# Performance work log

Hardware: AMD Instinct MI355X
Metric: run time of the kernel (lower is better)

Reference implementation:

```python
import jax, jax.numpy as jnp
import numpy as np

L, D, H, FF = 6, 1024, 16, 4096
HD = D // H
EPS = 1e-5


def _ln(x, g, b):
    m = jnp.mean(x, axis=-1, keepdims=True)
    v = jnp.var(x, axis=-1, keepdims=True)
    return (x - m) * jax.lax.rsqrt(v + EPS) * g + b


def _heads(t, S, B):  # [S,B,D] -> [B*H,S,HD]
    return t.reshape(S, B * H, HD).swapaxes(0, 1)


def _attn(q, k, v, mask):
    # q,k,v: [B*H, Sq/Sk, HD]; q pre-scaled
    scores = jnp.einsum('bqd,bkd->bqk', q, k)
    if mask is not None:
        scores = scores + mask  # broadcast [1,Sq,Sk]
    p = jax.nn.softmax(scores, axis=-1)
    return jnp.einsum('bqk,bkd->bqd', p, v)


def _self_attn(x, w_qkv, b_qkv, w_out, b_out, mask):
    S, B, _ = x.shape
    qkv = x @ w_qkv.T + b_qkv  # [S,B,3D]
    q, k, v = jnp.split(qkv, 3, axis=-1)
    q = q * (HD ** -0.5)
    a = _attn(_heads(q, S, B), _heads(k, S, B), _heads(v, S, B), mask)
    a = a.swapaxes(0, 1).reshape(S, B, D)
    return a @ w_out.T + b_out


def _cross_attn(x, mem, w_q, b_q, w_kv, b_kv, w_out, b_out):
    S, B, _ = x.shape
    Sm = mem.shape[0]
    q = (x @ w_q.T + b_q) * (HD ** -0.5)
    kv = mem @ w_kv.T + b_kv  # [Sm,B,2D]
    k, v = jnp.split(kv, 2, axis=-1)
    a = _attn(_heads(q, S, B), _heads(k, Sm, B), _heads(v, Sm, B), None)
    a = a.swapaxes(0, 1).reshape(S, B, D)
    return a @ w_out.T + b_out


def _ffn(x, w1, b1, w2, b2):
    h = jax.nn.gelu(x @ w1.T + b1, approximate=False)
    return h @ w2.T + b2


def setup_inputs() -> dict:
    key = jax.random.key(0)
    ks = iter(jax.random.split(key, 64))
    def p(*shape, s=0.02):
        return (jax.random.normal(next(ks), shape, dtype=jnp.float32) * s)
    inp = {
        'src': jax.random.normal(next(ks), (512, 8, D), dtype=jnp.float32),
        'tgt': jax.random.normal(next(ks), (512, 8, D), dtype=jnp.float32),
        # encoder params (stacked over L layers)
        'enc_qkv_w': p(L, 3 * D, D), 'enc_qkv_b': p(L, 3 * D),
        'enc_out_w': p(L, D, D), 'enc_out_b': p(L, D),
        'enc_ln1_g': jnp.ones((L, D)), 'enc_ln1_b': jnp.zeros((L, D)),
        'enc_fc1_w': p(L, FF, D), 'enc_fc1_b': p(L, FF),
        'enc_fc2_w': p(L, D, FF), 'enc_fc2_b': p(L, D),
        'enc_ln2_g': jnp.ones((L, D)), 'enc_ln2_b': jnp.zeros((L, D)),
        'enc_norm_g': jnp.ones((D,)), 'enc_norm_b': jnp.zeros((D,)),
        # decoder params
        'dec_qkv_w': p(L, 3 * D, D), 'dec_qkv_b': p(L, 3 * D),
        'dec_sout_w': p(L, D, D), 'dec_sout_b': p(L, D),
        'dec_ln1_g': jnp.ones((L, D)), 'dec_ln1_b': jnp.zeros((L, D)),
        'dec_q_w': p(L, D, D), 'dec_q_b': p(L, D),
        'dec_kv_w': p(L, 2 * D, D), 'dec_kv_b': p(L, 2 * D),
        'dec_cout_w': p(L, D, D), 'dec_cout_b': p(L, D),
        'dec_ln2_g': jnp.ones((L, D)), 'dec_ln2_b': jnp.zeros((L, D)),
        'dec_fc1_w': p(L, FF, D), 'dec_fc1_b': p(L, FF),
        'dec_fc2_w': p(L, D, FF), 'dec_fc2_b': p(L, D),
        'dec_ln3_g': jnp.ones((L, D)), 'dec_ln3_b': jnp.zeros((L, D)),
        'dec_norm_g': jnp.ones((D,)), 'dec_norm_b': jnp.zeros((D,)),
    }
    return inp


def reference(src, tgt,
              enc_qkv_w, enc_qkv_b, enc_out_w, enc_out_b,
              enc_ln1_g, enc_ln1_b, enc_fc1_w, enc_fc1_b,
              enc_fc2_w, enc_fc2_b, enc_ln2_g, enc_ln2_b,
              enc_norm_g, enc_norm_b,
              dec_qkv_w, dec_qkv_b, dec_sout_w, dec_sout_b,
              dec_ln1_g, dec_ln1_b, dec_q_w, dec_q_b,
              dec_kv_w, dec_kv_b, dec_cout_w, dec_cout_b,
              dec_ln2_g, dec_ln2_b, dec_fc1_w, dec_fc1_b,
              dec_fc2_w, dec_fc2_b, dec_ln3_g, dec_ln3_b,
              dec_norm_g, dec_norm_b):
    St = tgt.shape[0]
    # causal additive mask [1,St,St]
    causal = jnp.where(jnp.tril(jnp.ones((St, St), dtype=bool)), 0.0, -jnp.inf)
    causal = causal[None].astype(src.dtype)

    # ---- encoder ----
    x = src
    for i in range(L):
        x = x + _self_attn(_ln(x, enc_ln1_g[i], enc_ln1_b[i]),
                           enc_qkv_w[i], enc_qkv_b[i], enc_out_w[i], enc_out_b[i], None)
        x = x + _ffn(_ln(x, enc_ln2_g[i], enc_ln2_b[i]),
                     enc_fc1_w[i], enc_fc1_b[i], enc_fc2_w[i], enc_fc2_b[i])
    memory = _ln(x, enc_norm_g, enc_norm_b)

    # ---- decoder ----
    y = tgt
    for i in range(L):
        y = y + _self_attn(_ln(y, dec_ln1_g[i], dec_ln1_b[i]),
                           dec_qkv_w[i], dec_qkv_b[i], dec_sout_w[i], dec_sout_b[i], causal)
        y = y + _cross_attn(_ln(y, dec_ln2_g[i], dec_ln2_b[i]), memory,
                            dec_q_w[i], dec_q_b[i], dec_kv_w[i], dec_kv_b[i],
                            dec_cout_w[i], dec_cout_b[i])
        y = y + _ffn(_ln(y, dec_ln3_g[i], dec_ln3_b[i]),
                     dec_fc1_w[i], dec_fc1_b[i], dec_fc2_w[i], dec_fc2_b[i])
    return _ln(y, dec_norm_g, dec_norm_b)
```

## Files before the change

### kernel.cpp

```cpp
#include <hip/hip_runtime.h>

typedef __attribute__((ext_vector_type(4))) float f32x4;
typedef __attribute__((ext_vector_type(8))) short short8;
typedef unsigned int u32;
typedef unsigned short u16;
typedef __attribute__((ext_vector_type(2))) u32 u32x2;
typedef __attribute__((ext_vector_type(4))) u32 u32x4;

#define DEV __device__ __forceinline__
#define SB0  __builtin_amdgcn_sched_barrier(0)
#define HBAR asm volatile("s_barrier" ::: "memory")

DEV u16 f2b(float f){
  u32 u = __builtin_bit_cast(u32, f);
  u32 r = u + 0x7fffu + ((u >> 16) & 1u);
  return (u16)(r >> 16);
}
DEV u32 pk2(float a, float b){ return (u32)f2b(a) | ((u32)f2b(b) << 16); }

DEV void gload16(const void* g, void* l){
  __builtin_amdgcn_global_load_lds((const __attribute__((address_space(1))) void*)g,
                                   (__attribute__((address_space(3))) void*)l, 16, 0, 0);
}
DEV u32 lds_addr(void* p){
  return (u32)(unsigned long long)(__attribute__((address_space(3))) char*)p;
}

__global__ __launch_bounds__(256) void cvt_k(const float* __restrict__ in,
                                             u16* __restrict__ out, int n8)
{
  int i = blockIdx.x*256 + threadIdx.x;
  const int stride = gridDim.x*256;
  for (; i < n8; i += stride){
    const float4 a = ((const float4*)in)[2*i];
    const float4 b = ((const float4*)in)[2*i+1];
    u32x4 r;
    r.x = pk2(a.x,a.y); r.y = pk2(a.z,a.w);
    r.z = pk2(b.x,b.y); r.w = pk2(b.z,b.w);
    ((u32x4*)out)[i] = r;
  }
}

template<int OUT_F32>
__global__ __launch_bounds__(256) void ln_k(const float* __restrict__ x,
    const float* __restrict__ gam, const float* __restrict__ bet,
    void* __restrict__ out)
{
  const int row = blockIdx.x, tid = threadIdx.x;
  const float4 v = ((const float4*)(x + row*1024))[tid];
  float s = (v.x + v.y) + (v.z + v.w);
  float q = (v.x*v.x + v.y*v.y) + (v.z*v.z + v.w*v.w);
  #pragma unroll
  for (int m = 1; m < 64; m <<= 1){ s += __shfl_xor(s, m); q += __shfl_xor(q, m); }
  __shared__ float ps[4], pq[4];
  if ((tid & 63) == 0){ ps[tid>>6] = s; pq[tid>>6] = q; }
  __syncthreads();
  s = (ps[0]+ps[1]) + (ps[2]+ps[3]);
  q = (pq[0]+pq[1]) + (pq[2]+pq[3]);
  const float mean = s * (1.f/1024.f);
  const float var  = q * (1.f/1024.f) - mean*mean;
  const float rstd = rsqrtf(var + 1e-5f);
  const float4 gg = ((const float4*)gam)[tid];
  const float4 bb = ((const float4*)bet)[tid];
  const float o0 = (v.x-mean)*rstd*gg.x + bb.x;
  const float o1 = (v.y-mean)*rstd*gg.y + bb.y;
  const float o2 = (v.z-mean)*rstd*gg.z + bb.z;
  const float o3 = (v.w-mean)*rstd*gg.w + bb.w;
  if (OUT_F32){
    float4 r; r.x=o0; r.y=o1; r.z=o2; r.w=o3;
    ((float4*)out)[row*256 + tid] = r;
  } else {
    u32x2 r; r.x = pk2(o0,o1); r.y = pk2(o2,o3);
    ((u32x2*)out)[row*256 + tid] = r;
  }
}

template<int DO_GELU>
__global__ __launch_bounds__(512,2) void gemm256_k(
    const u16* __restrict__ A, const u16* __restrict__ W,
    const float* __restrict__ bias, u16* __restrict__ Cout,
    int M, int N, int K)
{
  __shared__ char lds[131072];
  const int tid = threadIdx.x;
  const int lane = tid & 63, wid = tid >> 6;
  const int wr = wid >> 2, wc = wid & 3;
  const int g = lane >> 4, c16 = lane & 15;

  const u32 nwg = gridDim.x * gridDim.y;
  u32 flat = blockIdx.x + gridDim.x * blockIdx.y;
  {
    const u32 q = nwg >> 3, r = nwg & 7;
    const u32 xcd = flat & 7, idx = flat >> 3;
    flat = (xcd < r ? xcd*(q+1) : r*(q+1) + (xcd-r)*q) + idx;
  }
  const int m0 = (int)(flat % gridDim.x) * 256;
  const int n0 = (int)(flat / gridDim.x) * 256;

  f32x4 acc[8][4];
  #pragma unroll
  for (int m = 0; m < 8; m++)
    #pragma unroll
    for (int n = 0; n < 4; n++) acc[m][n] = (f32x4){0.f,0.f,0.f,0.f};

  const int srow = tid >> 3, schk = tid & 7;
  const int scg = schk ^ (srow & 7);
  const u16* aS = A + (size_t)(m0 + srow)*K + scg*8;
  const u16* wS = W + (size_t)(n0 + srow)*K + scg*8;

  auto SG = [&](const u16* base, int regionOff, int sb, int half, int i, int kk){
    gload16(base + (size_t)(half*128 + i*64)*K + kk,
            lds + sb*65536 + regionOff + half*16384 + i*8192 + tid*16);
  };
  short8 af[4][2], bf[4][2];
  auto LDA4 = [&](char* bufA, int mbase){
    #pragma unroll
    for (int i = 0; i < 4; i++){
      const int r = (mbase + i)*16 + c16;
      const int rx = r & 7;
      af[i][0] = *(const short8*)(bufA + r*128 + ((g ^ rx) << 4));
      af[i][1] = *(const short8*)(bufA + r*128 + (((4 + g) ^ rx) << 4));
    }
  };
  auto LDB2 = [&](char* bufB, int nbase){
    #pragma unroll
    for (int i = 0; i < 2; i++){
      const int r = (wc & 1)*64 + (nbase + i)*16 + c16;
      const int rx = r & 7;
      bf[nbase+i][0] = *(const short8*)(bufB + r*128 + ((g ^ rx) << 4));
      bf[nbase+i][1] = *(const short8*)(bufB + r*128 + (((4 + g) ^ rx) << 4));
    }
  };

  const int NT = K >> 6;
  SG(wS, 32768, 0, 0, 0, 0); SG(wS, 32768, 0, 0, 1, 0);
  SG(wS, 32768, 0, 1, 0, 0); SG(wS, 32768, 0, 1, 1, 0);
  SG(aS, 0,     0, 0, 0, 0); SG(aS, 0,     0, 0, 1, 0);
  SG(aS, 0,     0, 1, 0, 0); SG(aS, 0,     0, 1, 1, 0);
  asm volatile("s_waitcnt vmcnt(1)" ::: "memory");
  HBAR;

  for (int t = 0; t < NT; ++t){
    const int b = t & 1, sb = b ^ 1;
    const int skk = (t+1) << 6;
    const bool st = (t+1 < NT);
    char* bufA = lds + b*65536 + wr*16384;
    char* bufB = lds + b*65536 + 32768 + (wc >> 1)*16384;

    LDA4(bufA, 0); LDB2(bufB, 0);
    if (st){ SG(wS, 32768, sb, 0, 0, skk); SG(wS, 32768, sb, 0, 1, skk); }
    HBAR;
    asm volatile("s_waitcnt lgkmcnt(0)" ::: "memory"); SB0;
    __builtin_amdgcn_s_setprio(1);
    #pragma unroll
    for (int ks = 0; ks < 2; ks++)
      #pragma unroll
      for (int i = 0; i < 4; i++)
        #pragma unroll
        for (int j = 0; j < 2; j++)
          acc[i][j] = __builtin_amdgcn_mfma_f32_16x16x32_bf16(af[i][ks], bf[j][ks], acc[i][j], 0,0,0);
    __builtin_amdgcn_s_setprio(0);
    LDB2(bufB, 2);
    if (st){ SG(wS, 32768, sb, 1, 0, skk); SG(wS, 32768, sb, 1, 1, skk); }
    HBAR;
    asm volatile("s_waitcnt lgkmcnt(0)" ::: "memory"); SB0;
    __builtin_amdgcn_s_setprio(1);
    #pragma unroll
    for (int ks = 0; ks < 2; ks++)
      #pragma unroll
      for (int i = 0; i < 4; i++)
        #pragma unroll
        for (int j = 2; j < 4; j++)
          acc[i][j] = __builtin_amdgcn_mfma_f32_16x16x32_bf16(af[i][ks], bf[j][ks], acc[i][j], 0,0,0);
    __builtin_amdgcn_s_setprio(0);
    if (st) asm volatile("s_waitcnt vmcnt(4)" ::: "memory");
    else    asm volatile("s_waitcnt vmcnt(0)" ::: "memory");
    HBAR;
    LDA4(bufA, 4);
    if (st){ SG(aS, 0, sb, 0, 0, skk); SG(aS, 0, sb, 0, 1, skk); }
    asm volatile("s_waitcnt lgkmcnt(0)" ::: "memory"); SB0;
    __builtin_amdgcn_s_setprio(1);
    #pragma unroll
    for (int ks = 0; ks < 2; ks++)
      #pragma unroll
      for (int i = 0; i < 4; i++)
        #pragma unroll
        for (int j = 0; j < 2; j++)
          acc[4+i][j] = __builtin_amdgcn_mfma_f32_16x16x32_bf16(af[i][ks], bf[j][ks], acc[4+i][j], 0,0,0);
    __builtin_amdgcn_s_setprio(0);
    if (st){ SG(aS, 0, sb, 1, 0, skk); SG(aS, 0, sb, 1, 1, skk); }
    HBAR;
    __builtin_amdgcn_s_setprio(1);
    #pragma unroll
    for (int ks = 0; ks < 2; ks++)
      #pragma unroll
      for (int i = 0; i < 4; i++)
        #pragma unroll
        for (int j = 2; j < 4; j++)
          acc[4+i][j] = __builtin_amdgcn_mfma_f32_16x16x32_bf16(af[i][ks], bf[j][ks], acc[4+i][j], 0,0,0);
    __builtin_amdgcn_s_setprio(0);
    if (st) asm volatile("s_waitcnt vmcnt(1)" ::: "memory");
    HBAR;
  }

  #pragma unroll
  for (int n = 0; n < 4; n++){
    const int col = n0 + wc*64 + n*16 + c16;
    const float bv = bias[col];
    #pragma unroll
    for (int m = 0; m < 8; m++){
      const int rbase = m0 + wr*128 + m*16 + g*4;
      #pragma unroll
      for (int r = 0; r < 4; r++){
        float v = acc[m][n][r] + bv;
        if (DO_GELU) v = 0.5f*v*(1.f + erff(v*0.70710678118654752f));
        Cout[(size_t)(rbase + r)*N + col] = f2b(v);
      }
    }
  }
}

template<int DO_GELU, int DO_RES, int OUT_F32>
__global__ __launch_bounds__(256,2) void gemm_k(
    const u16* __restrict__ A, const u16* __restrict__ W,
    const float* __restrict__ bias, const float* __restrict__ res,
    void* __restrict__ Cout, int M, int N, int K)
{
  __shared__ char sA[16384];
  __shared__ char sB[16384];
  const int tid = threadIdx.x;
  const int lane = tid & 63, w = tid >> 6;
  const int wr = w >> 1, wc = w & 1;
  const int g = lane >> 4, c16 = lane & 15;

  const u32 nwg = gridDim.x * gridDim.y;
  u32 flat = blockIdx.x + gridDim.x * blockIdx.y;
  {
    const u32 q = nwg >> 3, r = nwg & 7;
    const u32 xcd = flat & 7, idx = flat >> 3;
    flat = (xcd < r ? xcd*(q+1) : r*(q+1) + (xcd-r)*q) + idx;
  }
  const int m0 = (int)(flat % gridDim.x) * 128;
  const int n0 = (int)(flat / gridDim.x) * 128;

  f32x4 acc[4][4];
  #pragma unroll
  for (int m = 0; m < 4; m++)
    #pragma unroll
    for (int n = 0; n < 4; n++) acc[m][n] = (f32x4){0.f,0.f,0.f,0.f};

  const int arow = tid >> 3, achk = tid & 7;
  const int acg = achk ^ (arow & 7);
  const u16* aSrc = A + (size_t)(m0 + arow)*K + acg*8;
  const u16* wSrc = W + (size_t)(n0 + arow)*K + acg*8;
  char* aDst = sA + w*1024;
  char* bDst = sB + w*1024;

  for (int kk = 0; kk < K; kk += 64){
    __syncthreads();
    #pragma unroll
    for (int i = 0; i < 4; i++){
      gload16(aSrc + (size_t)i*32*K + kk, aDst + i*4096);
      gload16(wSrc + (size_t)i*32*K + kk, bDst + i*4096);
    }
    __syncthreads();
    #pragma unroll
    for (int ks = 0; ks < 2; ks++){
      short8 af[4], bf[4];
      #pragma unroll
      for (int m = 0; m < 4; m++){
        const int row = wr*64 + m*16 + c16;
        af[m] = *(const short8*)(sA + row*128 + (((ks*4 + g) ^ (row & 7)) << 4));
      }
      #pragma unroll
      for (int n = 0; n < 4; n++){
        const int row = wc*64 + n*16 + c16;
        bf[n] = *(const short8*)(sB + row*128 + (((ks*4 + g) ^ (row & 7)) << 4));
      }
      #pragma unroll
      for (int m = 0; m < 4; m++)
        #pragma unroll
        for (int n = 0; n < 4; n++)
          acc[m][n] = __builtin_amdgcn_mfma_f32_16x16x32_bf16(af[m], bf[n], acc[m][n], 0,0,0);
    }
  }
  #pragma unroll
  for (int n = 0; n < 4; n++){
    const int col = n0 + wc*64 + n*16 + c16;
    const float bv = bias[col];
    #pragma unroll
    for (int m = 0; m < 4; m++){
      const int rbase = m0 + wr*64 + m*16 + g*4;
      #pragma unroll
      for (int r = 0; r < 4; r++){
        float v = acc[m][n][r] + bv;
        if (DO_GELU) v = 0.5f*v*(1.f + erff(v*0.70710678118654752f));
        if (DO_RES)  v += res[(size_t)(rbase + r)*N + col];
        if (OUT_F32) ((float*)Cout)[(size_t)(rbase + r)*N + col] = v;
        else         ((u16*)Cout)[(size_t)(rbase + r)*N + col] = f2b(v);
      }
    }
  }
}

template<int DO_GELU, int DO_RES, int OUT_F32>
__global__ __launch_bounds__(256,2) void gemm64_k(
    const u16* __restrict__ A, const u16* __restrict__ W,
    const float* __restrict__ bias, const float* __restrict__ res,
    void* __restrict__ Cout, int M, int N, int K)
{
  __shared__ char sA[8192];
  __shared__ char sB[8192];
  const int tid = threadIdx.x;
  const int lane = tid & 63, w = tid >> 6;
  const int wr = w >> 1, wc = w & 1;
  const int g = lane >> 4, c16 = lane & 15;

  const u32 nwg = gridDim.x * gridDim.y;
  u32 flat = blockIdx.x + gridDim.x * blockIdx.y;
  {
    const u32 q = nwg >> 3, r = nwg & 7;
    const u32 xcd = flat & 7, idx = flat >> 3;
    flat = (xcd < r ? xcd*(q+1) : r*(q+1) + (xcd-r)*q) + idx;
  }
  const int m0 = (int)(flat % gridDim.x) * 64;
  const int n0 = (int)(flat / gridDim.x) * 64;

  f32x4 acc[2][2];
  #pragma unroll
  for (int m = 0; m < 2; m++)
    #pragma unroll
    for (int n = 0; n < 2; n++) acc[m][n] = (f32x4){0.f,0.f,0.f,0.f};

  const int arow = tid >> 3, achk = tid & 7;
  const int acg = achk ^ (arow & 7);
  const u16* aSrc = A + (size_t)(m0 + arow)*K + acg*8;
  const u16* wSrc = W + (size_t)(n0 + arow)*K + acg*8;
  char* aDst = sA + w*1024;
  char* bDst = sB + w*1024;

  for (int kk = 0; kk < K; kk += 64){
    __syncthreads();
    #pragma unroll
    for (int i = 0; i < 2; i++){
      gload16(aSrc + (size_t)i*32*K + kk, aDst + i*4096);
      gload16(wSrc + (size_t)i*32*K + kk, bDst + i*4096);
    }
    __syncthreads();
    #pragma unroll
    for (int ks = 0; ks < 2; ks++){
      short8 af[2], bf[2];
      #pragma unroll
      for (int m = 0; m < 2; m++){
        const int row = wr*32 + m*16 + c16;
        af[m] = *(const short8*)(sA + row*128 + (((ks*4 + g) ^ (row & 7)) << 4));
      }
      #pragma unroll
      for (int n = 0; n < 2; n++){
        const int row = wc*32 + n*16 + c16;
        bf[n] = *(const short8*)(sB + row*128 + (((ks*4 + g) ^ (row & 7)) << 4));
      }
      #pragma unroll
      for (int m = 0; m < 2; m++)
        #pragma unroll
        for (int n = 0; n < 2; n++)
          acc[m][n] = __builtin_amdgcn_mfma_f32_16x16x32_bf16(af[m], bf[n], acc[m][n], 0,0,0);
    }
  }
  #pragma unroll
  for (int n = 0; n < 2; n++){
    const int col = n0 + wc*32 + n*16 + c16;
    const float bv = bias[col];
    #pragma unroll
    for (int m = 0; m < 2; m++){
      const int rbase = m0 + wr*32 + m*16 + g*4;
      #pragma unroll
      for (int r = 0; r < 4; r++){
        float v = acc[m][n][r] + bv;
        if (DO_GELU) v = 0.5f*v*(1.f + erff(v*0.70710678118654752f));
        if (DO_RES)  v += res[(size_t)(rbase + r)*N + col];
        if (OUT_F32) ((float*)Cout)[(size_t)(rbase + r)*N + col] = v;
        else         ((u16*)Cout)[(size_t)(rbase + r)*N + col] = f2b(v);
      }
    }
  }
}

template<int CAUSAL>
__global__ __launch_bounds__(256,2) void attn_k(
    const u16* __restrict__ Qb, int qB, int qS,
    const u16* __restrict__ Kb, int kB, int kS,
    const u16* __restrict__ Vb, int vB, int vS,
    u16* __restrict__ Ob, int oB, int oS, float scale)
{
  __shared__ char smem[16384];
  const int tid = threadIdx.x;
  const int lane = tid & 63, w = tid >> 6;
  const int g = lane >> 4, c16 = lane & 15;
  const int qt = blockIdx.x, bh = blockIdx.y;
  const int b = bh >> 4, h = bh & 15;
  const u16* Q  = Qb + b*qB + h*64;
  const u16* Kp = Kb + b*kB + h*64;
  const u16* Vp = Vb + b*vB + h*64;
  u16*       Op = Ob + b*oB + h*64;

  const int qrow = qt*64 + w*16 + c16;
  const short8 bq0 = *(const short8*)(Q + qrow*qS + g*8);
  const short8 bq1 = *(const short8*)(Q + qrow*qS + 32 + g*8);

  f32x4 o[4];
  #pragma unroll
  for (int d = 0; d < 4; d++) o[d] = (f32x4){0.f,0.f,0.f,0.f};
  float mrun = -__builtin_inff(), lrun = 0.f;

  const int srow = tid >> 3, schk = tid & 7;
  const u16* kSrc = Kp + srow*kS + (schk ^ (srow & 7))*8;
  const u16* vSrc = Vp + srow*vS + schk*8;
  const u32 vtr0 = lds_addr(smem) + 8192 + (8*g + (c16 >> 2))*128 + (c16 & 3)*8;

  auto STAGE = [&](int p, int j0){
    gload16(kSrc + (size_t)j0*kS, smem + p*4096 + w*1024);
    gload16(vSrc + (size_t)j0*vS, smem + 8192 + p*4096 + w*1024);
  };
  auto COMPUTE = [&](int p, int j0){
    char* Ks = smem + p*4096;
    f32x4 st[2];
    #pragma unroll
    for (int t = 0; t < 2; t++){
      const int row = t*16 + c16;
      const int rx = row & 7;
      const short8 ka0 = *(const short8*)(Ks + row*128 + ((g ^ rx) << 4));
      const short8 ka1 = *(const short8*)(Ks + row*128 + (((4 + g) ^ rx) << 4));
      f32x4 z = (f32x4){0.f,0.f,0.f,0.f};
      z = __builtin_amdgcn_mfma_f32_16x16x32_bf16(ka0, bq0, z, 0,0,0);
      z = __builtin_amdgcn_mfma_f32_16x16x32_bf16(ka1, bq1, z, 0,0,0);
      st[t] = z;
    }
    float mloc = -__builtin_inff();
    #pragma unroll
    for (int t = 0; t < 2; t++)
      #pragma unroll
      for (int r = 0; r < 4; r++){
        float sv = st[t][r]*scale;
        if (CAUSAL){ if (j0 + t*16 + g*4 + r > qrow) sv = -__builtin_inff(); }
        st[t][r] = sv;
        mloc = fmaxf(mloc, sv);
      }
    mloc = fmaxf(mloc, __shfl_xor(mloc, 16));
    mloc = fmaxf(mloc, __shfl_xor(mloc, 32));
    const float mnew = fmaxf(mrun, mloc);
    const float corr = __expf(mrun - mnew);
    float psum = 0.f;
    u32 pk00, pk01, pk10, pk11;
    {
      float p0 = __expf(st[0][0]-mnew), p1 = __expf(st[0][1]-mnew);
      float p2 = __expf(st[0][2]-mnew), p3 = __expf(st[0][3]-mnew);
      psum += (p0+p1) + (p2+p3);
      pk00 = pk2(p0,p1); pk01 = pk2(p2,p3);
      p0 = __expf(st[1][0]-mnew); p1 = __expf(st[1][1]-mnew);
      p2 = __expf(st[1][2]-mnew); p3 = __expf(st[1][3]-mnew);
      psum += (p0+p1) + (p2+p3);
      pk10 = pk2(p0,p1); pk11 = pk2(p2,p3);
    }
    psum += __shfl_xor(psum, 16);
    psum += __shfl_xor(psum, 32);
    lrun = lrun*corr + psum;
    mrun = mnew;
    #pragma unroll
    for (int d = 0; d < 4; d++){
      o[d][0]*=corr; o[d][1]*=corr; o[d][2]*=corr; o[d][3]*=corr;
    }
    const int sl0 = c16 | (((g << 1)     & 3) << 4);
    const int sl1 = c16 | ((((g << 1)+1) & 3) << 4);
    const u32 a00 = (u32)__shfl((int)pk00, sl0), a01 = (u32)__shfl((int)pk01, sl0);
    const u32 a02 = (u32)__shfl((int)pk00, sl1), a03 = (u32)__shfl((int)pk01, sl1);
    const u32 a10 = (u32)__shfl((int)pk10, sl0), a11 = (u32)__shfl((int)pk11, sl0);
    const u32 a12 = (u32)__shfl((int)pk10, sl1), a13 = (u32)__shfl((int)pk11, sl1);
    const bool hi = g >= 2;
    union { short8 s; u32 u[4]; } pb;
    pb.u[0] = hi ? a10 : a00;
    pb.u[1] = hi ? a11 : a01;
    pb.u[2] = hi ? a12 : a02;
    pb.u[3] = hi ? a13 : a03;

    const u32 vtr = vtr0 + p*4096;
    u32x2 t00,t01,t10,t11,t20,t21,t30,t31;
    asm volatile("ds_read_b64_tr_b16 %0, %1 offset:0"   : "=v"(t00) : "v"(vtr));
    asm volatile("ds_read_b64_tr_b16 %0, %1 offset:512" : "=v"(t01) : "v"(vtr));
    asm volatile("ds_read_b64_tr_b16 %0, %1 offset:32"  : "=v"(t10) : "v"(vtr));
    asm volatile("ds_read_b64_tr_b16 %0, %1 offset:544" : "=v"(t11) : "v"(vtr));
    asm volatile("ds_read_b64_tr_b16 %0, %1 offset:64"  : "=v"(t20) : "v"(vtr));
    asm volatile("ds_read_b64_tr_b16 %0, %1 offset:576" : "=v"(t21) : "v"(vtr));
    asm volatile("ds_read_b64_tr_b16 %0, %1 offset:96"  : "=v"(t30) : "v"(vtr));
    asm volatile("ds_read_b64_tr_b16 %0, %1 offset:608" : "=v"(t31) : "v"(vtr));
    asm volatile("s_waitcnt lgkmcnt(0)" ::: "memory");
    __builtin_amdgcn_sched_barrier(0);
    union { short8 s; u32x2 d[2]; } v0u, v1u, v2u, v3u;
    v0u.d[0]=t00; v0u.d[1]=t01;
    v1u.d[0]=t10; v1u.d[1]=t11;
    v2u.d[0]=t20; v2u.d[1]=t21;
    v3u.d[0]=t30; v3u.d[1]=t31;
    o[0] = __builtin_amdgcn_mfma_f32_16x16x32_bf16(v0u.s, pb.s, o[0], 0,0,0);
    o[1] = __builtin_amdgcn_mfma_f32_16x16x32_bf16(v1u.s, pb.s, o[1], 0,0,0);
    o[2] = __builtin_amdgcn_mfma_f32_16x16x32_bf16(v2u.s, pb.s, o[2], 0,0,0);
    o[3] = __builtin_amdgcn_mfma_f32_16x16x32_bf16(v3u.s, pb.s, o[3], 0,0,0);
  };

  const int nCh = CAUSAL ? (2*qt + 2) : 16;
  STAGE(0, 0);
  for (int jc = 0; jc < nCh - 1; ++jc){
    STAGE((jc+1) & 1, (jc+1)*32);
    asm volatile("s_waitcnt vmcnt(2)" ::: "memory");
    HBAR; SB0;
    COMPUTE(jc & 1, jc*32);
    SB0; HBAR;
  }
  asm volatile("s_waitcnt vmcnt(0)" ::: "memory");
  HBAR; SB0;
  COMPUTE((nCh-1) & 1, (nCh-1)*32);
  SB0; HBAR;

  const float inv = 1.f / lrun;
  char* Olds = smem;
  #pragma unroll
  for (int dd = 0; dd < 4; dd++){
    u32x2 val;
    val.x = pk2(o[dd][0]*inv, o[dd][1]*inv);
    val.y = pk2(o[dd][2]*inv, o[dd][3]*inv);
    const int row = w*16 + c16;
    const int off = 32*dd + 8*g;
    const int chunk = off >> 4, rem = off & 15;
    *(u32x2*)(Olds + row*128 + ((chunk ^ (row & 7)) << 4) + rem) = val;
  }
  __syncthreads();
  const int orow = tid >> 2, oc = tid & 3;
  #pragma unroll
  for (int i = 0; i < 2; i++){
    const int ch = oc*2 + i;
    const u32x4 vv = *(const u32x4*)(Olds + orow*128 + ((ch ^ (orow & 7)) << 4));
    *(u32x4*)(Op + (qt*64 + orow)*oS + ch*8) = vv;
  }
}

static inline int cvt_grid(int n8){ int g = (n8 + 255) / 256; return g > 2048 ? 2048 : g; }

extern "C" void kernel_launch(void* const* d_in, const int* in_sizes, int n_in,
                              void* d_out, int out_size, void* d_ws, size_t ws_size,
                              hipStream_t stream)
{
  (void)in_sizes; (void)n_in; (void)out_size; (void)ws_size;
  const float* src      = (const float*)d_in[0];
  const float* tgt      = (const float*)d_in[1];
  const float* e_qkv_w  = (const float*)d_in[2];
  const float* e_qkv_b  = (const float*)d_in[3];
  const float* e_out_w  = (const float*)d_in[4];
  const float* e_out_b  = (const float*)d_in[5];
  const float* e_ln1_g  = (const float*)d_in[6];
  const float* e_ln1_b  = (const float*)d_in[7];
  const float* e_fc1_w  = (const float*)d_in[8];
  const float* e_fc1_b  = (const float*)d_in[9];
  const float* e_fc2_w  = (const float*)d_in[10];
  const float* e_fc2_b  = (const float*)d_in[11];
  const float* e_ln2_g  = (const float*)d_in[12];
  const float* e_ln2_b  = (const float*)d_in[13];
  const float* e_nrm_g  = (const float*)d_in[14];
  const float* e_nrm_b  = (const float*)d_in[15];
  const float* dc_qkv_w = (const float*)d_in[16];
  const float* dc_qkv_b = (const float*)d_in[17];
  const float* dc_sout_w= (const float*)d_in[18];
  const float* dc_sout_b= (const float*)d_in[19];
  const float* dc_ln1_g = (const float*)d_in[20];
  const float* dc_ln1_b = (const float*)d_in[21];
  const float* dc_q_w   = (const float*)d_in[22];
  const float* dc_q_b   = (const float*)d_in[23];
  const float* dc_kv_w  = (const float*)d_in[24];
  const float* dc_kv_b  = (const float*)d_in[25];
  const float* dc_cout_w= (const float*)d_in[26];
  const float* dc_cout_b= (const float*)d_in[27];
  const float* dc_ln2_g = (const float*)d_in[28];
  const float* dc_ln2_b = (const float*)d_in[29];
  const float* dc_fc1_w = (const float*)d_in[30];
  const float* dc_fc1_b = (const float*)d_in[31];
  const float* dc_fc2_w = (const float*)d_in[32];
  const float* dc_fc2_b = (const float*)d_in[33];
  const float* dc_ln3_g = (const float*)d_in[34];
  const float* dc_ln3_b = (const float*)d_in[35];
  const float* dc_nrm_g = (const float*)d_in[36];
  const float* dc_nrm_b = (const float*)d_in[37];

  char* ws = (char*)d_ws;
  u16*  ln_out = (u16*)(ws);
  u16*  attn_o = (u16*)(ws + (8u<<20));
  u16*  membuf = (u16*)(ws + (16u<<20));
  float* xres  = (float*)(ws + (24u<<20));
  u16*  region = (u16*)(ws + (40u<<20));
  u16*  qkv   = region;
  u16*  hbuf  = region;
  u16*  qbuf  = region;
  u16*  kvbuf = region + (4u<<20);

  const dim3 blk(256);
  const dim3 blk512(512);
  const int M = 4096;

  u16* wb = (u16*)(ws + (72u<<20));
  size_t woff = 0;
  auto CV = [&](const float* wsrc, size_t n)->u16* {
    u16* p = wb + woff; woff += n;
    cvt_k<<<cvt_grid((int)(n >> 3)), blk, 0, stream>>>(wsrc, p, (int)(n >> 3));
    return p;
  };
  u16* Weqkv = CV(e_qkv_w,  6ull*3072*1024);
  u16* Weout = CV(e_out_w,  6ull*1024*1024);
  u16* Wefc1 = CV(e_fc1_w,  6ull*4096*1024);
  u16* Wefc2 = CV(e_fc2_w,  6ull*4096*1024);
  u16* Wdqkv = CV(dc_qkv_w, 6ull*3072*1024);
  u16* Wdsout= CV(dc_sout_w,6ull*1024*1024);
  u16* Wdq   = CV(dc_q_w,   6ull*1024*1024);
  u16* Wdkv  = CV(dc_kv_w,  6ull*2048*1024);
  u16* Wdcout= CV(dc_cout_w,6ull*1024*1024);
  u16* Wdfc1 = CV(dc_fc1_w, 6ull*4096*1024);
  u16* Wdfc2 = CV(dc_fc2_w, 6ull*4096*1024);

  for (int i = 0; i < 6; i++){
    const float* xin = i ? xres : src;
    ln_k<0><<<4096, blk, 0, stream>>>(xin, e_ln1_g + i*1024, e_ln1_b + i*1024, ln_out);
    gemm256_k<0><<<dim3(16, 12), blk512, 0, stream>>>(ln_out,
        Weqkv + (size_t)i*3145728, e_qkv_b + i*3072, qkv, M, 3072, 1024);
    attn_k<0><<<dim3(8,128), blk, 0, stream>>>(qkv, 3072, 24576,
        qkv+1024, 3072, 24576, qkv+2048, 3072, 24576, attn_o, 1024, 8192, 0.125f);
    gemm64_k<0,1,1><<<dim3(64, 16), blk, 0, stream>>>(attn_o,
        Weout + (size_t)i*1048576, e_out_b + i*1024, xin, xres, M, 1024, 1024);
    ln_k<0><<<4096, blk, 0, stream>>>(xres, e_ln2_g + i*1024, e_ln2_b + i*1024, ln_out);
    gemm256_k<1><<<dim3(16, 16), blk512, 0, stream>>>(ln_out,
        Wefc1 + (size_t)i*4194304, e_fc1_b + i*4096, hbuf, M, 4096, 1024);
    gemm64_k<0,1,1><<<dim3(64, 16), blk, 0, stream>>>(hbuf,
        Wefc2 + (size_t)i*4194304, e_fc2_b + i*1024, xres, xres, M, 1024, 4096);
  }
  ln_k<0><<<4096, blk, 0, stream>>>(xres, e_nrm_g, e_nrm_b, membuf);

  for (int i = 0; i < 6; i++){
    const float* yin = i ? xres : tgt;
    ln_k<0><<<4096, blk, 0, stream>>>(yin, dc_ln1_g + i*1024, dc_ln1_b + i*1024, ln_out);
    gemm256_k<0><<<dim3(16, 12), blk512, 0, stream>>>(ln_out,
        Wdqkv + (size_t)i*3145728, dc_qkv_b + i*3072, qkv, M, 3072, 1024);
    attn_k<1><<<dim3(8,128), blk, 0, stream>>>(qkv, 3072, 24576,
        qkv+1024, 3072, 24576, qkv+2048, 3072, 24576, attn_o, 1024, 8192, 0.125f);
    gemm64_k<0,1,1><<<dim3(64, 16), blk, 0, stream>>>(attn_o,
        Wdsout + (size_t)i*1048576, dc_sout_b + i*1024, yin, xres, M, 1024, 1024);
    ln_k<0><<<4096, blk, 0, stream>>>(xres, dc_ln2_g + i*1024, dc_ln2_b + i*1024, ln_out);
    gemm64_k<0,0,0><<<dim3(64, 16), blk, 0, stream>>>(ln_out,
        Wdq + (size_t)i*1048576, dc_q_b + i*1024, nullptr, qbuf, M, 1024, 1024);
    gemm64_k<0,0,0><<<dim3(64, 32), blk, 0, stream>>>(membuf,
        Wdkv + (size_t)i*2097152, dc_kv_b + i*2048, nullptr, kvbuf, M, 2048, 1024);
    attn_k<0><<<dim3(8,128), blk, 0, stream>>>(qbuf, 1024, 8192,
        kvbuf, 2048, 16384, kvbuf+1024, 2048, 16384, attn_o, 1024, 8192, 0.125f);
    gemm64_k<0,1,1><<<dim3(64, 16), blk, 0, stream>>>(attn_o,
        Wdcout + (size_t)i*1048576, dc_cout_b + i*1024, xres, xres, M, 1024, 1024);
    ln_k<0><<<4096, blk, 0, stream>>>(xres, dc_ln3_g + i*1024, dc_ln3_b + i*1024, ln_out);
    gemm256_k<1><<<dim3(16, 16), blk512, 0, stream>>>(ln_out,
        Wdfc1 + (size_t)i*4194304, dc_fc1_b + i*4096, hbuf, M, 4096, 1024);
    gemm64_k<0,1,1><<<dim3(64, 16), blk, 0, stream>>>(hbuf,
        Wdfc2 + (size_t)i*4194304, dc_fc2_b + i*1024, xres, xres, M, 1024, 4096);
  }
  ln_k<1><<<4096, blk, 0, stream>>>(xres, dc_nrm_g, dc_nrm_b, d_out);
}
```

Baseline: 3.615 ms.

## Replace 64x64 GEMM with double-buffered 128x128 pipelined 8-wave kernel

Replaces the 64x64-tile single-buffered GEMM used for the N=1024/2048 projections with a new 128x128-tile kernel that uses 512 threads (8 waves), double-buffered LDS (64KB), and prefetches the next K-tile via global_load_lds while computing on the current one. It uses explicit waitcnt and barriers, splits A-fragment loads into two halves, and raises MFMA priority with setprio. The aim is to hide global-load latency and improve data reuse per tile. In exchange the grid drops to 256 or 512 workgroups, which may underfill the GPU's compute units for the 1024-wide outputs.

```diff
diff --git a/kernel.cpp b/kernel.cpp
--- a/kernel.cpp
+++ b/kernel.cpp
@@ -221,16 +221,15 @@
 }
 
 template<int DO_GELU, int DO_RES, int OUT_F32>
-__global__ __launch_bounds__(256,2) void gemm_k(
+__global__ __launch_bounds__(512,2) void gemm128p_k(
     const u16* __restrict__ A, const u16* __restrict__ W,
     const float* __restrict__ bias, const float* __restrict__ res,
     void* __restrict__ Cout, int M, int N, int K)
 {
-  __shared__ char sA[16384];
-  __shared__ char sB[16384];
+  __shared__ char lds[65536];
   const int tid = threadIdx.x;
-  const int lane = tid & 63, w = tid >> 6;
-  const int wr = w >> 1, wc = w & 1;
+  const int lane = tid & 63, wid = tid >> 6;
+  const int wr = wid >> 2, wc = wid & 3;
   const int g = lane >> 4, c16 = lane & 15;
 
   const u32 nwg = gridDim.x * gridDim.y;
@@ -243,137 +242,89 @@
   const int m0 = (int)(flat % gridDim.x) * 128;
   const int n0 = (int)(flat / gridDim.x) * 128;
 
-  f32x4 acc[4][4];
+  f32x4 acc[4][2];
   #pragma unroll
   for (int m = 0; m < 4; m++)
     #pragma unroll
-    for (int n = 0; n < 4; n++) acc[m][n] = (f32x4){0.f,0.f,0.f,0.f};
-
-  const int arow = tid >> 3, achk = tid & 7;
-  const int acg = achk ^ (arow & 7);
-  const u16* aSrc = A + (size_t)(m0 + arow)*K + acg*8;
-  const u16* wSrc = W + (size_t)(n0 + arow)*K + acg*8;
-  char* aDst = sA + w*1024;
-  char* bDst = sB + w*1024;
-
-  for (int kk = 0; kk < K; kk += 64){
-    __syncthreads();
-    #pragma unroll
-    for (int i = 0; i < 4; i++){
-      gload16(aSrc + (size_t)i*32*K + kk, aDst + i*4096);
-      gload16(wSrc + (size_t)i*32*K + kk, bDst + i*4096);
-    }
-    __syncthreads();
-    #pragma unroll
-    for (int ks = 0; ks < 2; ks++){
-      short8 af[4], bf[4];
-      #pragma unroll
-      for (int m = 0; m < 4; m++){
-        const int row = wr*64 + m*16 + c16;
-        af[m] = *(const short8*)(sA + row*128 + (((ks*4 + g) ^ (row & 7)) << 4));
-      }
-      #pragma unroll
-      for (int n = 0; n < 4; n++){
-        const int row = wc*64 + n*16 + c16;
-        bf[n] = *(const short8*)(sB + row*128 + (((ks*4 + g) ^ (row & 7)) << 4));
-      }
-      #pragma unroll
-      for (int m = 0; m < 4; m++)
+    for (int n = 0; n < 2; n++) acc[m][n] = (f32x4){0.f,0.f,0.f,0.f};
+
+  const int srow = tid >> 3, schk = tid & 7;
+  const int scg = schk ^ (srow & 7);
+  const u16* aS = A + (size_t)(m0 + srow)*K + scg*8;
+  const u16* wS = W + (size_t)(n0 + srow)*K + scg*8;
+
+  auto SG = [&](const u16* base, int regionOff, int sb, int i, int kk){
+    gload16(base + (size_t)(i*64)*K + kk,
+            lds + sb*32768 + regionOff + i*8192 + tid*16);
+  };
+  short8 af[2][2], af2[2][2], bf[2][2];
+  auto LDA = [&](short8 (*dst)[2], char* bufA, int mbase){
+    #pragma unroll
+    for (int i = 0; i < 2; i++){
+      const int r = wr*64 + (mbase + i)*16 + c16;
+      const int rx = r & 7;
+      dst[i][0] = *(const short8*)(bufA + r*128 + ((g ^ rx) << 4));
+      dst[i][1] = *(const short8*)(bufA + r*128 + (((4 + g) ^ rx) << 4));
+    }
+  };
+  auto LDB = [&](char* bufB){
+    #pragma unroll
+    for (int i = 0; i < 2; i++){
+      const int r = wc*32 + i*16 + c16;
+      const int rx = r & 7;
+      bf[i][0] = *(const short8*)(bufB + r*128 + ((g ^ rx) << 4));
+      bf[i][1] = *(const short8*)(bufB + r*128 + (((4 + g) ^ rx) << 4));
+    }
+  };
+
+  const int NT = K >> 6;
+  SG(wS, 16384, 0, 0, 0); SG(wS, 16384, 0, 1, 0);
+  SG(aS, 0,     0, 0, 0); SG(aS, 0,     0, 1, 0);
+
+  for (int t = 0; t < NT; ++t){
+    const int b = t & 1, sb = b ^ 1;
+    const int skk = (t+1) << 6;
+    const bool st = (t+1 < NT);
+    char* bufA = lds + b*32768;
+    char* bufB = lds + b*32768 + 16384;
+
+    if (st){ SG(wS, 16384, sb, 0, skk); SG(wS, 16384, sb, 1, skk); }
+    if (st) asm volatile("s_waitcnt vmcnt(2)" ::: "memory");
+    else    asm volatile("s_waitcnt vmcnt(0)" ::: "memory");
+    HBAR;
+    LDA(af, bufA, 0); LDB(bufB);
+    if (st){ SG(aS, 0, sb, 0, skk); SG(aS, 0, sb, 1, skk); }
+    asm volatile("s_waitcnt lgkmcnt(0)" ::: "memory"); SB0;
+    __builtin_amdgcn_s_setprio(1);
+    #pragma unroll
+    for (int ks = 0; ks < 2; ks++)
+      #pragma unroll
+      for (int i = 0; i < 2; i++)
         #pragma unroll
-        for (int n = 0; n < 4; n++)
-          acc[m][n] = __builtin_amdgcn_mfma_f32_16x16x32_bf16(af[m], bf[n], acc[m][n], 0,0,0);
-    }
-  }
-  #pragma unroll
-  for (int n = 0; n < 4; n++){
-    const int col = n0 + wc*64 + n*16 + c16;
-    const float bv = bias[col];
-    #pragma unroll
-    for (int m = 0; m < 4; m++){
-      const int rbase = m0 + wr*64 + m*16 + g*4;
-      #pragma unroll
-      for (int r = 0; r < 4; r++){
-        float v = acc[m][n][r] + bv;
-        if (DO_GELU) v = 0.5f*v*(1.f + erff(v*0.70710678118654752f));
-        if (DO_RES)  v += res[(size_t)(rbase + r)*N + col];
-        if (OUT_F32) ((float*)Cout)[(size_t)(rbase + r)*N + col] = v;
-        else         ((u16*)Cout)[(size_t)(rbase + r)*N + col] = f2b(v);
-      }
-    }
-  }
-}
-
-template<int DO_GELU, int DO_RES, int OUT_F32>
-__global__ __launch_bounds__(256,2) void gemm64_k(
-    const u16* __restrict__ A, const u16* __restrict__ W,
-    const float* __restrict__ bias, const float* __restrict__ res,
-    void* __restrict__ Cout, int M, int N, int K)
-{
-  __shared__ char sA[8192];
-  __shared__ char sB[8192];
-  const int tid = threadIdx.x;
-  const int lane = tid & 63, w = tid >> 6;
-  const int wr = w >> 1, wc = w & 1;
-  const int g = lane >> 4, c16 = lane & 15;
-
-  const u32 nwg = gridDim.x * gridDim.y;
-  u32 flat = blockIdx.x + gridDim.x * blockIdx.y;
-  {
-    const u32 q = nwg >> 3, r = nwg & 7;
-    const u32 xcd = flat & 7, idx = flat >> 3;
-    flat = (xcd < r ? xcd*(q+1) : r*(q+1) + (xcd-r)*q) + idx;
-  }
-  const int m0 = (int)(flat % gridDim.x) * 64;
-  const int n0 = (int)(flat / gridDim.x) * 64;
-
-  f32x4 acc[2][2];
-  #pragma unroll
-  for (int m = 0; m < 2; m++)
-    #pragma unroll
-    for (int n = 0; n < 2; n++) acc[m][n] = (f32x4){0.f,0.f,0.f,0.f};
-
-  const int arow = tid >> 3, achk = tid & 7;
-  const int acg = achk ^ (arow & 7);
-  const u16* aSrc = A + (size_t)(m0 + arow)*K + acg*8;
-  const u16* wSrc = W + (size_t)(n0 + arow)*K + acg*8;
-  char* aDst = sA + w*1024;
-  char* bDst = sB + w*1024;
-
-  for (int kk = 0; kk < K; kk += 64){
-    __syncthreads();
-    #pragma unroll
-    for (int i = 0; i < 2; i++){
-      gload16(aSrc + (size_t)i*32*K + kk, aDst + i*4096);
-      gload16(wSrc + (size_t)i*32*K + kk, bDst + i*4096);
-    }
-    __syncthreads();
-    #pragma unroll
-    for (int ks = 0; ks < 2; ks++){
-      short8 af[2], bf[2];
-      #pragma unroll
-      for (int m = 0; m < 2; m++){
-        const int row = wr*32 + m*16 + c16;
-        af[m] = *(const short8*)(sA + row*128 + (((ks*4 + g) ^ (row & 7)) << 4));
-      }
-      #pragma unroll
-      for (int n = 0; n < 2; n++){
-        const int row = wc*32 + n*16 + c16;
-        bf[n] = *(const short8*)(sB + row*128 + (((ks*4 + g) ^ (row & 7)) << 4));
-      }
-      #pragma unroll
-      for (int m = 0; m < 2; m++)
+        for (int j = 0; j < 2; j++)
+          acc[i][j] = __builtin_amdgcn_mfma_f32_16x16x32_bf16(af[i][ks], bf[j][ks], acc[i][j], 0,0,0);
+    __builtin_amdgcn_s_setprio(0);
+    LDA(af2, bufA, 2);
+    asm volatile("s_waitcnt lgkmcnt(0)" ::: "memory"); SB0;
+    __builtin_amdgcn_s_setprio(1);
+    #pragma unroll
+    for (int ks = 0; ks < 2; ks++)
+      #pragma unroll
+      for (int i = 0; i < 2; i++)
         #pragma unroll
-        for (int n = 0; n < 2; n++)
-          acc[m][n] = __builtin_amdgcn_mfma_f32_16x16x32_bf16(af[m], bf[n], acc[m][n], 0,0,0);
-    }
-  }
+        for (int j = 0; j < 2; j++)
+          acc[2+i][j] = __builtin_amdgcn_mfma_f32_16x16x32_bf16(af2[i][ks], bf[j][ks], acc[2+i][j], 0,0,0);
+    __builtin_amdgcn_s_setprio(0);
+    HBAR;
+  }
+
   #pragma unroll
   for (int n = 0; n < 2; n++){
     const int col = n0 + wc*32 + n*16 + c16;
     const float bv = bias[col];
     #pragma unroll
-    for (int m = 0; m < 2; m++){
-      const int rbase = m0 + wr*32 + m*16 + g*4;
+    for (int m = 0; m < 4; m++){
+      const int rbase = m0 + wr*64 + m*16 + g*4;
       #pragma unroll
       for (int r = 0; r < 4; r++){
         float v = acc[m][n][r] + bv;
@@ -629,12 +580,12 @@
         Weqkv + (size_t)i*3145728, e_qkv_b + i*3072, qkv, M, 3072, 1024);
     attn_k<0><<<dim3(8,128), blk, 0, stream>>>(qkv, 3072, 24576,
         qkv+1024, 3072, 24576, qkv+2048, 3072, 24576, attn_o, 1024, 8192, 0.125f);
-    gemm64_k<0,1,1><<<dim3(64, 16), blk, 0, stream>>>(attn_o,
+    gemm128p_k<0,1,1><<<dim3(32, 8), blk512, 0, stream>>>(attn_o,
         Weout + (size_t)i*1048576, e_out_b + i*1024, xin, xres, M, 1024, 1024);
     ln_k<0><<<4096, blk, 0, stream>>>(xres, e_ln2_g + i*1024, e_ln2_b + i*1024, ln_out);
     gemm256_k<1><<<dim3(16, 16), blk512, 0, stream>>>(ln_out,
         Wefc1 + (size_t)i*4194304, e_fc1_b + i*4096, hbuf, M, 4096, 1024);
-    gemm64_k<0,1,1><<<dim3(64, 16), blk, 0, stream>>>(hbuf,
+    gemm128p_k<0,1,1><<<dim3(32, 8), blk512, 0, stream>>>(hbuf,
         Wefc2 + (size_t)i*4194304, e_fc2_b + i*1024, xres, xres, M, 1024, 4096);
   }
   ln_k<0><<<4096, blk, 0, stream>>>(xres, e_nrm_g, e_nrm_b, membuf);
@@ -646,21 +597,21 @@
         Wdqkv + (size_t)i*3145728, dc_qkv_b + i*3072, qkv, M, 3072, 1024);
     attn_k<1><<<dim3(8,128), blk, 0, stream>>>(qkv, 3072, 24576,
         qkv+1024, 3072, 24576, qkv+2048, 3072, 24576, attn_o, 1024, 8192, 0.125f);
-    gemm64_k<0,1,1><<<dim3(64, 16), blk, 0, stream>>>(attn_o,
+    gemm128p_k<0,1,1><<<dim3(32, 8), blk512, 0, stream>>>(attn_o,
         Wdsout + (size_t)i*1048576, dc_sout_b + i*1024, yin, xres, M, 1024, 1024);
     ln_k<0><<<4096, blk, 0, stream>>>(xres, dc_ln2_g + i*1024, dc_ln2_b + i*1024, ln_out);
-    gemm64_k<0,0,0><<<dim3(64, 16), blk, 0, stream>>>(ln_out,
+    gemm128p_k<0,0,0><<<dim3(32, 8), blk512, 0, stream>>>(ln_out,
         Wdq + (size_t)i*1048576, dc_q_b + i*1024, nullptr, qbuf, M, 1024, 1024);
-    gemm64_k<0,0,0><<<dim3(64, 32), blk, 0, stream>>>(membuf,
+    gemm128p_k<0,0,0><<<dim3(32, 16), blk512, 0, stream>>>(membuf,
         Wdkv + (size_t)i*2097152, dc_kv_b + i*2048, nullptr, kvbuf, M, 2048, 1024);
     attn_k<0><<<dim3(8,128), blk, 0, stream>>>(qbuf, 1024, 8192,
         kvbuf, 2048, 16384, kvbuf+1024, 2048, 16384, attn_o, 1024, 8192, 0.125f);
-    gemm64_k<0,1,1><<<dim3(64, 16), blk, 0, stream>>>(attn_o,
+    gemm128p_k<0,1,1><<<dim3(32, 8), blk512, 0, stream>>>(attn_o,
         Wdcout + (size_t)i*1048576, dc_cout_b + i*1024, xres, xres, M, 1024, 1024);
     ln_k<0><<<4096, blk, 0, stream>>>(xres, dc_ln3_g + i*1024, dc_ln3_b + i*1024, ln_out);
     gemm256_k<1><<<dim3(16, 16), blk512, 0, stream>>>(ln_out,
         Wdfc1 + (size_t)i*4194304, dc_fc1_b + i*4096, hbuf, M, 4096, 1024);
-    gemm64_k<0,1,1><<<dim3(64, 16), blk, 0, stream>>>(hbuf,
+    gemm128p_k<0,1,1><<<dim3(32, 8), blk512, 0, stream>>>(hbuf,
         Wdfc2 + (size_t)i*4194304, dc_fc2_b + i*1024, xres, xres, M, 1024, 4096);
   }
   ln_k<1><<<4096, blk, 0, stream>>>(xres, dc_nrm_g, dc_nrm_b, d_out);
```

Result: faster. 3.266 ms (-9.7%).
